# Optimization experiments

Measured on AMD Instinct MI355X. Metric: run time of the kernel, lower is better.

Reference implementation:

```python
import jax, jax.numpy as jnp
import numpy as np

N_NODES = 100000


def gcn_conv(x, W, b, src, dst, n_nodes):
    """PyG-style GCNConv: add self-loops, symmetric normalization, aggregate to dst."""
    x = x @ W  # [N, out]
    loop = jnp.arange(n_nodes, dtype=src.dtype)
    src_sl = jnp.concatenate([src, loop])  # [E+N]
    dst_sl = jnp.concatenate([dst, loop])
    deg = jax.ops.segment_sum(jnp.ones(src_sl.shape[0], x.dtype), dst_sl,
                              num_segments=n_nodes)  # [N]
    dinv = jnp.where(deg > 0, jax.lax.rsqrt(deg), 0.0)
    norm = dinv[src_sl] * dinv[dst_sl]  # [E+N]
    msg = x[src_sl] * norm[:, None]  # gather + scale
    out = jax.ops.segment_sum(msg, dst_sl, num_segments=n_nodes)  # scatter-add
    return out + b


def setup_inputs() -> dict:
    key = jax.random.key(0)
    ks = jax.random.split(key, 8)
    in_d, hid_d, out_d = 64, 128, 64
    x = jax.random.normal(ks[0], (N_NODES, in_d), dtype=jnp.float32)
    edge_index = jax.random.randint(ks[1], (2, 1000000), 0, N_NODES, dtype=jnp.int64)
    s1 = 1.0 / np.sqrt(in_d)
    s2 = 1.0 / np.sqrt(hid_d)
    sc = 1.0 / np.sqrt(2 * out_d)
    W1 = jax.random.uniform(ks[2], (in_d, hid_d), jnp.float32, -s1, s1)
    b1 = jnp.zeros((hid_d,), jnp.float32)
    W2 = jax.random.uniform(ks[3], (hid_d, out_d), jnp.float32, -s2, s2)
    b2 = jnp.zeros((out_d,), jnp.float32)
    Wc = jax.random.uniform(ks[4], (2 * out_d, 1), jnp.float32, -sc, sc)
    bc = jax.random.uniform(ks[5], (1,), jnp.float32, -sc, sc)
    return {"x": x, "edge_index": edge_index, "W1": W1, "b1": b1,
            "W2": W2, "b2": b2, "Wc": Wc, "bc": bc}


def reference(x, edge_index, W1, b1, W2, b2, Wc, bc):
    src, dst = edge_index[0], edge_index[1]
    h = jax.nn.relu(gcn_conv(x, W1, b1, src, dst, N_NODES))
    h = jax.nn.relu(gcn_conv(h, W2, b2, src, dst, N_NODES))
    # edge-level gather-concat-linear-sigmoid
    edge_emb = jnp.concatenate([h[src], h[dst]], axis=1)  # [E, 2*out_d]
    logits = edge_emb @ Wc + bc  # [E, 1]
    return jax.nn.sigmoid(logits)
```

## Files before the change

### kernel.cpp

```cpp
#include <hip/hip_runtime.h>
#include <hip/hip_fp16.h>
#include <math.h>

#define IN_D 64
#define HID_D 128
#define OUT_D 64

typedef _Float16 half8 __attribute__((ext_vector_type(8)));
typedef float f32x4 __attribute__((ext_vector_type(4)));

#define ECAP   16384
#define CSRCAP (ECAP + 512 * 7)
#define DCHUNK 2048

__global__ void k_init(int* __restrict__ bcur,
                       const float* __restrict__ W1, const float* __restrict__ W2,
                       __half* __restrict__ w1f, __half* __restrict__ w2f,
                       __half* __restrict__ xs, __half* __restrict__ ts,
                       int N, int nbuk) {
    int t = blockIdx.x * 256 + threadIdx.x;
    if (blockIdx.x == 0 && threadIdx.x < nbuk)
        bcur[threadIdx.x] = threadIdx.x * ECAP;
    if (t < 2048) {
        int which = t >> 10, fl = t & 1023;
        int f = fl >> 6, l = fl & 63, q = l >> 4, n16 = l & 15;
        if (which == 0) {
            int nt = f >> 1, kc = f & 1, n = nt * 16 + n16, k0 = kc * 32 + q * 8;
            for (int j = 0; j < 8; ++j)
                w1f[(size_t)fl * 8 + j] = __float2half(W1[(k0 + j) * 128 + n]);
        } else {
            int nt = f >> 2, kc = f & 3, n = nt * 16 + n16, k0 = kc * 32 + q * 8;
            for (int j = 0; j < 8; ++j)
                w2f[(size_t)fl * 8 + j] = __float2half(W2[(k0 + j) * 64 + n]);
        }
    } else {
        int si = t - 2048;
        if (si < 64) {
            xs[(size_t)N * 64 + si] = __float2half(0.f);
            ts[(size_t)N * 64 + si] = __float2half(0.f);
        }
    }
}

__global__ __launch_bounds__(256) void k_decode3(const unsigned int* __restrict__ raw,
                                                 int E,
                                                 int2* __restrict__ sd,
                                                 int* __restrict__ bcur,
                                                 int2* __restrict__ pairs) {
    __shared__ int hist[256];
    __shared__ int base[256];
    __shared__ int cnt[256];
    __shared__ int is64s;
    if (threadIdx.x == 0) {
        int f = 1;
        for (int i = 1; i < 64; i += 2) f &= (raw[i] == 0u);
        is64s = f;
    }
    hist[threadIdx.x] = 0; cnt[threadIdx.x] = 0;
    __syncthreads();
    int is64 = is64s;
    int e0 = blockIdx.x * DCHUNK;
    int s[8], d[8], b[8];
    if ((E & 1) == 0) {
#pragma unroll
        for (int i = 0; i < 4; ++i) {
            int e = e0 + (threadIdx.x + i * 256) * 2;
            if (e < E) {
                int s0, d0, s1, d1;
                if (is64) {
                    uint4 sv = *(const uint4*)&raw[2 * (size_t)e];
                    uint4 dv = *(const uint4*)&raw[2 * ((size_t)E + e)];
                    s0 = (int)sv.x; s1 = (int)sv.z;
                    d0 = (int)dv.x; d1 = (int)dv.z;
                } else {
                    uint2 sv = *(const uint2*)&raw[e];
                    uint2 dv = *(const uint2*)&raw[E + e];
                    s0 = (int)sv.x; s1 = (int)sv.y;
                    d0 = (int)dv.x; d1 = (int)dv.y;
                }
                *(int4*)&sd[e] = make_int4(s0, d0, s1, d1);
                s[2 * i] = s0; d[2 * i] = d0; b[2 * i] = d0 >> 9;
                s[2 * i + 1] = s1; d[2 * i + 1] = d1; b[2 * i + 1] = d1 >> 9;
                atomicAdd(&hist[b[2 * i]], 1);
                atomicAdd(&hist[b[2 * i + 1]], 1);
            } else { b[2 * i] = -1; b[2 * i + 1] = -1; }
        }
    } else {
#pragma unroll
        for (int i = 0; i < 8; ++i) {
            int e = e0 + threadIdx.x + i * 256;
            if (e < E) {
                int sv, dv;
                if (is64) {
                    sv = (int)raw[2 * (size_t)e];
                    dv = (int)raw[2 * ((size_t)E + e)];
                } else {
                    sv = (int)raw[e];
                    dv = (int)raw[E + e];
                }
                sd[e] = make_int2(sv, dv);
                s[i] = sv; d[i] = dv; b[i] = dv >> 9;
                atomicAdd(&hist[b[i]], 1);
            } else b[i] = -1;
        }
    }
    __syncthreads();
    if (hist[threadIdx.x] > 0)
        base[threadIdx.x] = atomicAdd(&bcur[threadIdx.x], hist[threadIdx.x]);
    __syncthreads();
#pragma unroll
    for (int i = 0; i < 8; ++i) {
        if (b[i] >= 0) {
            int pos = base[b[i]] + atomicAdd(&cnt[b[i]], 1);
            pairs[pos] = make_int2(s[i], d[i]);
        }
    }
}

__global__ __launch_bounds__(256) void k_build(const int2* __restrict__ pairs,
                                               const int* __restrict__ bcur,
                                               int2* __restrict__ prowdeg,
                                               int* __restrict__ csr_src,
                                               float* __restrict__ dinv,
                                               const float* __restrict__ x,
                                               __half* __restrict__ xs,
                                               int N) {
    __shared__ int deg5[512];
    __shared__ int cur5[512];
    __shared__ int wsum[4];
    int b = blockIdx.x;
    int n0 = b << 9;
    int n1 = n0 + 512; if (n1 > N) n1 = N;
    int nn = n1 - n0;
    deg5[threadIdx.x] = 0;
    deg5[threadIdx.x + 256] = 0;
    __syncthreads();
    int beg = b * ECAP, end = bcur[b];
    for (int i = beg + threadIdx.x; i < end; i += 256)
        atomicAdd(&deg5[pairs[i].y - n0], 1);
    __syncthreads();
    int pbase = b * CSRCAP;
    int t = threadIdx.x;
    int v0 = deg5[2 * t], v1 = deg5[2 * t + 1];
    int p0 = (v0 + 7) & ~7, p1 = (v1 + 7) & ~7;
    int s = p0 + p1;
    int lane = t & 63, w = t >> 6;
    int inc = s;
    for (int off = 1; off < 64; off <<= 1) {
        int n = __shfl_up(inc, off);
        if (lane >= off) inc += n;
    }
    if (lane == 63) wsum[w] = inc;
    __syncthreads();
    for (int k = 0; k < w; ++k) inc += wsum[k];
    int ex0 = inc - s, ex1 = inc - p1;
    int ps0 = pbase + ex0, ps1 = pbase + ex1;
    cur5[2 * t] = ps0;
    cur5[2 * t + 1] = ps1;
    if (2 * t < nn) {
        prowdeg[n0 + 2 * t] = make_int2(ps0, p0);
        dinv[n0 + 2 * t] = rsqrtf((float)v0 + 1.0f);
    }
    if (2 * t + 1 < nn) {
        prowdeg[n0 + 2 * t + 1] = make_int2(ps1, p1);
        dinv[n0 + 2 * t + 1] = rsqrtf((float)v1 + 1.0f);
    }
    __syncthreads();
    for (int i = beg + threadIdx.x; i < end; i += 256) {
        int2 r = pairs[i];
        int pos = atomicAdd(&cur5[r.y - n0], 1);
        csr_src[pos] = r.x;
    }
    __syncthreads();
    for (int i = cur5[2 * t]; i < ps0 + p0; ++i) csr_src[i] = N;
    for (int i = cur5[2 * t + 1]; i < ps1 + p1; ++i) csr_src[i] = N;
    for (int idx = t; idx < nn * 8; idx += 256) {
        int i = idx >> 3, c8 = (idx & 7) * 8;
        int node = n0 + i;
        float di = rsqrtf((float)deg5[i] + 1.0f);
        float4 va = *(const float4*)&x[(size_t)node * 64 + c8];
        float4 vb = *(const float4*)&x[(size_t)node * 64 + c8 + 4];
        union { __half2 h[4]; uint4 u; } pk2;
        pk2.h[0] = __floats2half2_rn(va.x * di, va.y * di);
        pk2.h[1] = __floats2half2_rn(va.z * di, va.w * di);
        pk2.h[2] = __floats2half2_rn(vb.x * di, vb.y * di);
        pk2.h[3] = __floats2half2_rn(vb.z * di, vb.w * di);
        *(uint4*)&xs[(size_t)node * 64 + c8] = pk2.u;
    }
}

__global__ __launch_bounds__(256) void k_gather1(const __half* __restrict__ xs,
                          const float* __restrict__ dinv,
                          const int2* __restrict__ prowdeg, const int* __restrict__ csr,
                          __half* __restrict__ agg, int N) {
    int wv = threadIdx.x >> 6, l = threadIdx.x & 63;
    int ns = l >> 4, slot = (l >> 3) & 1, seg = l & 7;
    int node = (blockIdx.x * 4 + wv) * 4 + ns;
    bool valid = node < N;
    int nc = valid ? node : N - 1;
    int2 rp = prowdeg[nc];
    int beg = rp.x;
    int pend = beg + (valid ? rp.y : 0);
    float di = dinv[nc];
    half8 hs = *(const half8*)&xs[(size_t)nc * 64 + seg * 8];
    float acc[8];
#pragma unroll
    for (int j = 0; j < 8; ++j) acc[j] = 0.f;
    for (int k = beg + slot; k < pend; k += 8) {
        int s0 = csr[k], s1 = csr[k + 2], s2 = csr[k + 4], s3 = csr[k + 6];
        half8 h0 = *(const half8*)&xs[(size_t)s0 * 64 + seg * 8];
        half8 h1 = *(const half8*)&xs[(size_t)s1 * 64 + seg * 8];
        half8 h2 = *(const half8*)&xs[(size_t)s2 * 64 + seg * 8];
        half8 h3 = *(const half8*)&xs[(size_t)s3 * 64 + seg * 8];
#pragma unroll
        for (int j = 0; j < 8; ++j) {
            float t01 = (float)h0[j] + (float)h1[j];
            float t23 = (float)h2[j] + (float)h3[j];
            acc[j] += t01 + t23;
        }
    }
#pragma unroll
    for (int j = 0; j < 8; ++j) acc[j] += __shfl_xor(acc[j], 8);
    if (slot == 0 && valid) {
        half8 o;
#pragma unroll
        for (int j = 0; j < 8; ++j) o[j] = (_Float16)((acc[j] + (float)hs[j]) * di);
        *(half8*)&agg[(size_t)node * 64 + seg * 8] = o;
    }
}

__global__ __launch_bounds__(256) void k_gather2(const __half* __restrict__ ts,
                          const float* __restrict__ dinv,
                          const int2* __restrict__ prowdeg, const int* __restrict__ csr,
                          const float* __restrict__ b2, const float* __restrict__ Wc,
                          float* __restrict__ s0o, float* __restrict__ s1o, int N) {
    int wv = threadIdx.x >> 6, l = threadIdx.x & 63;
    int ns = l >> 4, slot = (l >> 3) & 1, seg = l & 7;
    int node = (blockIdx.x * 4 + wv) * 4 + ns;
    bool valid = node < N;
    int nc = valid ? node : N - 1;
    int2 rp = prowdeg[nc];
    int beg = rp.x;
    int pend = beg + (valid ? rp.y : 0);
    float di = dinv[nc];
    half8 hs = *(const half8*)&ts[(size_t)nc * 64 + seg * 8];
    float acc[8];
#pragma unroll
    for (int j = 0; j < 8; ++j) acc[j] = 0.f;
    for (int k = beg + slot; k < pend; k += 8) {
        int s0 = csr[k], s1 = csr[k + 2], s2 = csr[k + 4], s3 = csr[k + 6];
        half8 h0 = *(const half8*)&ts[(size_t)s0 * 64 + seg * 8];
        half8 h1 = *(const half8*)&ts[(size_t)s1 * 64 + seg * 8];
        half8 h2 = *(const half8*)&ts[(size_t)s2 * 64 + seg * 8];
        half8 h3 = *(const half8*)&ts[(size_t)s3 * 64 + seg * 8];
#pragma unroll
        for (int j = 0; j < 8; ++j) {
            float t01 = (float)h0[j] + (float)h1[j];
            float t23 = (float)h2[j] + (float)h3[j];
            acc[j] += t01 + t23;
        }
    }
#pragma unroll
    for (int j = 0; j < 8; ++j) acc[j] += __shfl_xor(acc[j], 8);
    if (slot == 0) {
        float4 b2a = *(const float4*)&b2[seg * 8];
        float4 b2b = *(const float4*)&b2[seg * 8 + 4];
        float4 w0a = *(const float4*)&Wc[seg * 8];
        float4 w0b = *(const float4*)&Wc[seg * 8 + 4];
        float4 w1a = *(const float4*)&Wc[64 + seg * 8];
        float4 w1b = *(const float4*)&Wc[64 + seg * 8 + 4];
        float bb[8] = {b2a.x, b2a.y, b2a.z, b2a.w, b2b.x, b2b.y, b2b.z, b2b.w};
        float w0[8] = {w0a.x, w0a.y, w0a.z, w0a.w, w0b.x, w0b.y, w0b.z, w0b.w};
        float w1[8] = {w1a.x, w1a.y, w1a.z, w1a.w, w1b.x, w1b.y, w1b.z, w1b.w};
        float p0 = 0.f, p1 = 0.f;
#pragma unroll
        for (int j = 0; j < 8; ++j) {
            float v = fmaxf((acc[j] + (float)hs[j]) * di + bb[j], 0.f);
            p0 = fmaf(v, w0[j], p0);
            p1 = fmaf(v, w1[j], p1);
        }
        p0 += __shfl_xor(p0, 1); p1 += __shfl_xor(p1, 1);
        p0 += __shfl_xor(p0, 2); p1 += __shfl_xor(p1, 2);
        p0 += __shfl_xor(p0, 4); p1 += __shfl_xor(p1, 4);
        if (seg == 0 && valid) { s0o[node] = p0; s1o[node] = p1; }
    }
}

__global__ __launch_bounds__(256) void k_mlp_mfma(const __half* __restrict__ agg_h,
                                                  const __half* __restrict__ w1f,
                                                  const __half* __restrict__ w2f,
                                                  const float* __restrict__ b1,
                                                  const float* __restrict__ dinv,
                                                  __half* __restrict__ ts, int N) {
    __shared__ __align__(16) __half w1l[8192];
    __shared__ __align__(16) __half w2l[8192];
    {
        const float4* sA = (const float4*)w1f;
        const float4* sB = (const float4*)w2f;
        float4* dA = (float4*)w1l;
        float4* dB = (float4*)w2l;
        for (int i = threadIdx.x; i < 1024; i += 256) { dA[i] = sA[i]; dB[i] = sB[i]; }
    }
    __syncthreads();

    int wv = threadIdx.x >> 6, l = threadIdx.x & 63;
    int m0 = blockIdx.x * 64 + wv * 16;
    if (m0 >= N) return;
    int q = l >> 4, ml = l & 15;
    int rowA = m0 + ml; if (rowA >= N) rowA = N - 1;

    half8 bfr0 = *(const half8*)&agg_h[(size_t)rowA * 64 + q * 8];
    half8 bfr1 = *(const half8*)&agg_h[(size_t)rowA * 64 + 32 + q * 8];

    int pk[8][2];
#pragma unroll
    for (int nt = 0; nt < 8; ++nt) {
        float4 bb = *(const float4*)&b1[nt * 16 + q * 4];
        f32x4 cacc; cacc[0] = bb.x; cacc[1] = bb.y; cacc[2] = bb.z; cacc[3] = bb.w;
        half8 a0 = *(const half8*)&w1l[(nt * 2 + 0) * 512 + l * 8];
        cacc = __builtin_amdgcn_mfma_f32_16x16x32_f16(a0, bfr0, cacc, 0, 0, 0);
        half8 a1 = *(const half8*)&w1l[(nt * 2 + 1) * 512 + l * 8];
        cacc = __builtin_amdgcn_mfma_f32_16x16x32_f16(a1, bfr1, cacc, 0, 0, 0);
        union { __half2 h; int i; } u0, u1;
        u0.h = __floats2half2_rn(fmaxf(cacc[0], 0.f), fmaxf(cacc[1], 0.f));
        u1.h = __floats2half2_rn(fmaxf(cacc[2], 0.f), fmaxf(cacc[3], 0.f));
        pk[nt][0] = u0.i;
        pk[nt][1] = u1.i;
    }

    int src0 = ml + 16 * ((2 * q) & 3);
    int src1 = ml + 16 * ((2 * q + 1) & 3);
    bool hi = (q >= 2);
    half8 afr[4];
#pragma unroll
    for (int kc = 0; kc < 4; ++kc) {
        int t0 = 2 * kc, t1 = 2 * kc + 1;
        int d0a = __shfl(pk[t0][0], src0), d0b = __shfl(pk[t1][0], src0);
        int d1a = __shfl(pk[t0][1], src0), d1b = __shfl(pk[t1][1], src0);
        int d2a = __shfl(pk[t0][0], src1), d2b = __shfl(pk[t1][0], src1);
        int d3a = __shfl(pk[t0][1], src1), d3b = __shfl(pk[t1][1], src1);
        union { int d[4]; half8 h; } u;
        u.d[0] = hi ? d0b : d0a;
        u.d[1] = hi ? d1b : d1a;
        u.d[2] = hi ? d2b : d2a;
        u.d[3] = hi ? d3b : d3a;
        afr[kc] = u.h;
    }

    float dl = dinv[rowA];
    float dv[4];
#pragma unroll
    for (int r = 0; r < 4; ++r) dv[r] = __shfl(dl, q * 4 + r);

#pragma unroll
    for (int nt2 = 0; nt2 < 4; ++nt2) {
        f32x4 cacc; cacc[0] = 0.f; cacc[1] = 0.f; cacc[2] = 0.f; cacc[3] = 0.f;
#pragma unroll
        for (int kc = 0; kc < 4; ++kc) {
            half8 b = *(const half8*)&w2l[(nt2 * 4 + kc) * 512 + l * 8];
            cacc = __builtin_amdgcn_mfma_f32_16x16x32_f16(afr[kc], b, cacc, 0, 0, 0);
        }
#pragma unroll
        for (int r = 0; r < 4; ++r) {
            int node = m0 + q * 4 + r;
            if (node < N)
                ts[(size_t)node * 64 + nt2 * 16 + ml] = __float2half(cacc[r] * dv[r]);
        }
    }
}

__global__ void k_edge(const int2* __restrict__ sd,
                       const float* __restrict__ s0, const float* __restrict__ s1,
                       const float* __restrict__ bc, float* __restrict__ out, int E) {
    int e = (blockIdx.x * blockDim.x + threadIdx.x) * 2;
    if (e >= E) return;
    float b = bc[0];
    if (e + 1 < E) {
        int4 v = *(const int4*)&sd[e];
        float z0 = s0[v.x] + s1[v.y] + b;
        float z1 = s0[v.z] + s1[v.w] + b;
        float2 o;
        o.x = 1.0f / (1.0f + __expf(-z0));
        o.y = 1.0f / (1.0f + __expf(-z1));
        *(float2*)&out[e] = o;
    } else {
        int2 v = sd[e];
        float z = s0[v.x] + s1[v.y] + b;
        out[e] = 1.0f / (1.0f + __expf(-z));
    }
}

extern "C" void kernel_launch(void* const* d_in, const int* in_sizes, int n_in,
                              void* d_out, int out_size, void* d_ws, size_t ws_size,
                              hipStream_t stream) {
    const float* x  = (const float*)d_in[0];
    const unsigned int* eidx = (const unsigned int*)d_in[1];
    const float* W1 = (const float*)d_in[2];
    const float* b1 = (const float*)d_in[3];
    const float* W2 = (const float*)d_in[4];
    const float* b2 = (const float*)d_in[5];
    const float* Wc = (const float*)d_in[6];
    const float* bc = (const float*)d_in[7];
    float* out = (float*)d_out;

    int N = in_sizes[0] / IN_D;
    int E = in_sizes[1] / 2;
    int nbuk = (N + 511) >> 9;
    int nchunk = (E + DCHUNK - 1) / DCHUNK;

    char* p = (char*)d_ws;
    int2*  sd      = (int2*)p;   p += (size_t)E * 8;
    int*   bcur    = (int*)p;    p += 256 * 4;
    int*   csr_src = (int*)p;    p += (size_t)nbuk * CSRCAP * 4;
    float* dinv    = (float*)p;  p += (size_t)N * 4;
    float* s0      = (float*)p;  p += (size_t)N * 4;
    float* s1      = (float*)p;  p += (size_t)N * 4;
    p += 15; p = (char*)((size_t)p & ~(size_t)15);
    int2*  prowdeg = (int2*)p;   p += (size_t)N * 8;
    int2*  pairs   = (int2*)p;   p += (size_t)nbuk * ECAP * 8;
    __half* xs    = (__half*)p;  p += (size_t)(N + 1) * 64 * 2;
    __half* aggh  = (__half*)p;  p += (size_t)N * 64 * 2;
    __half* ts    = (__half*)p;  p += (size_t)(N + 1) * 64 * 2;
    __half* w1f   = (__half*)p;  p += 8192 * 2;
    __half* w2f   = (__half*)p;  p += 8192 * 2;

    k_init<<<9, 256, 0, stream>>>(bcur, W1, W2, w1f, w2f, xs, ts, N, nbuk);
    k_decode3<<<nchunk, 256, 0, stream>>>(eidx, E, sd, bcur, pairs);
    k_build<<<nbuk, 256, 0, stream>>>(pairs, bcur, prowdeg, csr_src, dinv, x, xs, N);

    k_gather1<<<(N + 15) / 16, 256, 0, stream>>>(xs, dinv, prowdeg, csr_src, aggh, N);

    k_mlp_mfma<<<(N + 63) / 64, 256, 0, stream>>>(aggh, w1f, w2f, b1, dinv, ts, N);

    k_gather2<<<(N + 15) / 16, 256, 0, stream>>>(ts, dinv, prowdeg, csr_src,
                                                 b2, Wc, s0, s1, N);

    k_edge<<<(E / 2 + 255) / 256, 256, 0, stream>>>(sd, s0, s1, bc, out, E);
}
```

Before: 191.2 us.

## Drop sd edge buffer, read raw indices in edge kernel, single-slot gathers

Removes the intermediate sd array written by the decode kernel. The edge kernel now reads src/dst directly from the raw int64/int32 edge_index, which saves an 8MB write plus its readback. CSR row padding drops from multiples of 8 to multiples of 4. The gather kernels now handle 8 nodes per wave, one lane group per node, load 4 neighbor indices with a single int4 read, and no longer need the cross-slot shuffle reduction. The trade-off is less memory-level parallelism per node and more loop iterations for high-degree nodes. The edge kernel also reads the wider raw int64 indices.

```diff
diff --git a/kernel.cpp b/kernel.cpp
--- a/kernel.cpp
+++ b/kernel.cpp
@@ -10,7 +10,7 @@
 typedef float f32x4 __attribute__((ext_vector_type(4)));
 
 #define ECAP   16384
-#define CSRCAP (ECAP + 512 * 7)
+#define CSRCAP (ECAP + 512 * 3)
 #define DCHUNK 2048
 
 __global__ void k_init(int* __restrict__ bcur,
@@ -44,7 +44,6 @@
 
 __global__ __launch_bounds__(256) void k_decode3(const unsigned int* __restrict__ raw,
                                                  int E,
-                                                 int2* __restrict__ sd,
                                                  int* __restrict__ bcur,
                                                  int2* __restrict__ pairs) {
     __shared__ int hist[256];
@@ -78,7 +77,6 @@
                     s0 = (int)sv.x; s1 = (int)sv.y;
                     d0 = (int)dv.x; d1 = (int)dv.y;
                 }
-                *(int4*)&sd[e] = make_int4(s0, d0, s1, d1);
                 s[2 * i] = s0; d[2 * i] = d0; b[2 * i] = d0 >> 9;
                 s[2 * i + 1] = s1; d[2 * i + 1] = d1; b[2 * i + 1] = d1 >> 9;
                 atomicAdd(&hist[b[2 * i]], 1);
@@ -98,7 +96,6 @@
                     sv = (int)raw[e];
                     dv = (int)raw[E + e];
                 }
-                sd[e] = make_int2(sv, dv);
                 s[i] = sv; d[i] = dv; b[i] = dv >> 9;
                 atomicAdd(&hist[b[i]], 1);
             } else b[i] = -1;
@@ -142,7 +139,7 @@
     int pbase = b * CSRCAP;
     int t = threadIdx.x;
     int v0 = deg5[2 * t], v1 = deg5[2 * t + 1];
-    int p0 = (v0 + 7) & ~7, p1 = (v1 + 7) & ~7;
+    int p0 = (v0 + 3) & ~3, p1 = (v1 + 3) & ~3;
     int s = p0 + p1;
     int lane = t & 63, w = t >> 6;
     int inc = s;
@@ -194,8 +191,8 @@
                           const int2* __restrict__ prowdeg, const int* __restrict__ csr,
                           __half* __restrict__ agg, int N) {
     int wv = threadIdx.x >> 6, l = threadIdx.x & 63;
-    int ns = l >> 4, slot = (l >> 3) & 1, seg = l & 7;
-    int node = (blockIdx.x * 4 + wv) * 4 + ns;
+    int ns = l >> 3, seg = l & 7;
+    int node = (blockIdx.x * 4 + wv) * 8 + ns;
     bool valid = node < N;
     int nc = valid ? node : N - 1;
     int2 rp = prowdeg[nc];
@@ -206,12 +203,12 @@
     float acc[8];
 #pragma unroll
     for (int j = 0; j < 8; ++j) acc[j] = 0.f;
-    for (int k = beg + slot; k < pend; k += 8) {
-        int s0 = csr[k], s1 = csr[k + 2], s2 = csr[k + 4], s3 = csr[k + 6];
-        half8 h0 = *(const half8*)&xs[(size_t)s0 * 64 + seg * 8];
-        half8 h1 = *(const half8*)&xs[(size_t)s1 * 64 + seg * 8];
-        half8 h2 = *(const half8*)&xs[(size_t)s2 * 64 + seg * 8];
-        half8 h3 = *(const half8*)&xs[(size_t)s3 * 64 + seg * 8];
+    for (int k = beg; k < pend; k += 4) {
+        int4 s4 = *(const int4*)&csr[k];
+        half8 h0 = *(const half8*)&xs[(size_t)s4.x * 64 + seg * 8];
+        half8 h1 = *(const half8*)&xs[(size_t)s4.y * 64 + seg * 8];
+        half8 h2 = *(const half8*)&xs[(size_t)s4.z * 64 + seg * 8];
+        half8 h3 = *(const half8*)&xs[(size_t)s4.w * 64 + seg * 8];
 #pragma unroll
         for (int j = 0; j < 8; ++j) {
             float t01 = (float)h0[j] + (float)h1[j];
@@ -219,9 +216,7 @@
             acc[j] += t01 + t23;
         }
     }
-#pragma unroll
-    for (int j = 0; j < 8; ++j) acc[j] += __shfl_xor(acc[j], 8);
-    if (slot == 0 && valid) {
+    if (valid) {
         half8 o;
 #pragma unroll
         for (int j = 0; j < 8; ++j) o[j] = (_Float16)((acc[j] + (float)hs[j]) * di);
@@ -235,8 +230,8 @@
                           const float* __restrict__ b2, const float* __restrict__ Wc,
                           float* __restrict__ s0o, float* __restrict__ s1o, int N) {
     int wv = threadIdx.x >> 6, l = threadIdx.x & 63;
-    int ns = l >> 4, slot = (l >> 3) & 1, seg = l & 7;
-    int node = (blockIdx.x * 4 + wv) * 4 + ns;
+    int ns = l >> 3, seg = l & 7;
+    int node = (blockIdx.x * 4 + wv) * 8 + ns;
     bool valid = node < N;
     int nc = valid ? node : N - 1;
     int2 rp = prowdeg[nc];
@@ -247,12 +242,12 @@
     float acc[8];
 #pragma unroll
     for (int j = 0; j < 8; ++j) acc[j] = 0.f;
-    for (int k = beg + slot; k < pend; k += 8) {
-        int s0 = csr[k], s1 = csr[k + 2], s2 = csr[k + 4], s3 = csr[k + 6];
-        half8 h0 = *(const half8*)&ts[(size_t)s0 * 64 + seg * 8];
-        half8 h1 = *(const half8*)&ts[(size_t)s1 * 64 + seg * 8];
-        half8 h2 = *(const half8*)&ts[(size_t)s2 * 64 + seg * 8];
-        half8 h3 = *(const half8*)&ts[(size_t)s3 * 64 + seg * 8];
+    for (int k = beg; k < pend; k += 4) {
+        int4 s4 = *(const int4*)&csr[k];
+        half8 h0 = *(const half8*)&ts[(size_t)s4.x * 64 + seg * 8];
+        half8 h1 = *(const half8*)&ts[(size_t)s4.y * 64 + seg * 8];
+        half8 h2 = *(const half8*)&ts[(size_t)s4.z * 64 + seg * 8];
+        half8 h3 = *(const half8*)&ts[(size_t)s4.w * 64 + seg * 8];
 #pragma unroll
         for (int j = 0; j < 8; ++j) {
             float t01 = (float)h0[j] + (float)h1[j];
@@ -260,9 +255,7 @@
             acc[j] += t01 + t23;
         }
     }
-#pragma unroll
-    for (int j = 0; j < 8; ++j) acc[j] += __shfl_xor(acc[j], 8);
-    if (slot == 0) {
+    {
         float4 b2a = *(const float4*)&b2[seg * 8];
         float4 b2b = *(const float4*)&b2[seg * 8 + 4];
         float4 w0a = *(const float4*)&Wc[seg * 8];
@@ -369,24 +362,52 @@
     }
 }
 
-__global__ void k_edge(const int2* __restrict__ sd,
+__global__ void k_edge(const unsigned int* __restrict__ raw,
                        const float* __restrict__ s0, const float* __restrict__ s1,
                        const float* __restrict__ bc, float* __restrict__ out, int E) {
+    __shared__ int is64s;
+    if (threadIdx.x == 0) {
+        int f = 1;
+        for (int i = 1; i < 64; i += 2) f &= (raw[i] == 0u);
+        is64s = f;
+    }
+    __syncthreads();
+    int is64 = is64s;
     int e = (blockIdx.x * blockDim.x + threadIdx.x) * 2;
     if (e >= E) return;
     float b = bc[0];
-    if (e + 1 < E) {
-        int4 v = *(const int4*)&sd[e];
-        float z0 = s0[v.x] + s1[v.y] + b;
-        float z1 = s0[v.z] + s1[v.w] + b;
+    if (((E & 1) == 0) && (e + 1 < E)) {
+        int sa, sb, da, db;
+        if (is64) {
+            uint4 sv = *(const uint4*)&raw[2 * (size_t)e];
+            uint4 dv = *(const uint4*)&raw[2 * ((size_t)E + e)];
+            sa = (int)sv.x; sb = (int)sv.z;
+            da = (int)dv.x; db = (int)dv.z;
+        } else {
+            uint2 sv = *(const uint2*)&raw[e];
+            uint2 dv = *(const uint2*)&raw[E + e];
+            sa = (int)sv.x; sb = (int)sv.y;
+            da = (int)dv.x; db = (int)dv.y;
+        }
+        float z0 = s0[sa] + s1[da] + b;
+        float z1 = s0[sb] + s1[db] + b;
         float2 o;
         o.x = 1.0f / (1.0f + __expf(-z0));
         o.y = 1.0f / (1.0f + __expf(-z1));
         *(float2*)&out[e] = o;
     } else {
-        int2 v = sd[e];
-        float z = s0[v.x] + s1[v.y] + b;
-        out[e] = 1.0f / (1.0f + __expf(-z));
+        for (int k = e; k < E && k < e + 2; ++k) {
+            int sa, da;
+            if (is64) {
+                sa = (int)raw[2 * (size_t)k];
+                da = (int)raw[2 * ((size_t)E + k)];
+            } else {
+                sa = (int)raw[k];
+                da = (int)raw[E + k];
+            }
+            float z = s0[sa] + s1[da] + b;
+            out[k] = 1.0f / (1.0f + __expf(-z));
+        }
     }
 }
 
@@ -409,7 +430,6 @@
     int nchunk = (E + DCHUNK - 1) / DCHUNK;
 
     char* p = (char*)d_ws;
-    int2*  sd      = (int2*)p;   p += (size_t)E * 8;
     int*   bcur    = (int*)p;    p += 256 * 4;
     int*   csr_src = (int*)p;    p += (size_t)nbuk * CSRCAP * 4;
     float* dinv    = (float*)p;  p += (size_t)N * 4;
@@ -425,15 +445,15 @@
     __half* w2f   = (__half*)p;  p += 8192 * 2;
 
     k_init<<<9, 256, 0, stream>>>(bcur, W1, W2, w1f, w2f, xs, ts, N, nbuk);
-    k_decode3<<<nchunk, 256, 0, stream>>>(eidx, E, sd, bcur, pairs);
+    k_decode3<<<nchunk, 256, 0, stream>>>(eidx, E, bcur, pairs);
     k_build<<<nbuk, 256, 0, stream>>>(pairs, bcur, prowdeg, csr_src, dinv, x, xs, N);
 
-    k_gather1<<<(N + 15) / 16, 256, 0, stream>>>(xs, dinv, prowdeg, csr_src, aggh, N);
+    k_gather1<<<(N + 31) / 32, 256, 0, stream>>>(xs, dinv, prowdeg, csr_src, aggh, N);
 
     k_mlp_mfma<<<(N + 63) / 64, 256, 0, stream>>>(aggh, w1f, w2f, b1, dinv, ts, N);
 
-    k_gather2<<<(N + 15) / 16, 256, 0, stream>>>(ts, dinv, prowdeg, csr_src,
+    k_gather2<<<(N + 31) / 32, 256, 0, stream>>>(ts, dinv, prowdeg, csr_src,
                                                  b2, Wc, s0, s1, N);
 
-    k_edge<<<(E / 2 + 255) / 256, 256, 0, stream>>>(sd, s0, s1, bc, out, E);
-}
+    k_edge<<<(E / 2 + 255) / 256, 256, 0, stream>>>(eidx, s0, s1, bc, out, E);
+}
```

After: 193.0 us. Within noise of the previous version (+1.0%).
